# Kernel tuning notes

Measured on AMD Instinct MI355X. Metric: run time of the kernel, lower is better.

Reference implementation:

```python
import jax, jax.numpy as jnp
import numpy as np

N_SRC, N_DST, E, D, H = 100000, 10000, 320000, 128, 128
LN_EPS = 1e-5


def setup_inputs() -> dict:
    key = jax.random.key(0)
    ks = jax.random.split(key, 12)
    h_src = jax.random.normal(ks[0], (N_SRC, D), jnp.float32)
    h_dst = jax.random.normal(ks[1], (N_DST, D), jnp.float32)
    s_emb = jax.random.normal(ks[2], (N_DST, D), jnp.float32)
    edge_weight = jax.random.uniform(ks[3], (E,), jnp.float32)
    src_idx = jax.random.randint(ks[4], (E,), 0, N_SRC)
    dst_idx = jnp.sort(jax.random.randint(ks[5], (E,), 0, N_DST))
    # session_attention: Linear(2D->H, no bias) -> tanh -> Linear(H->1, no bias)
    W1 = jax.random.normal(ks[6], (2 * D, H), jnp.float32) / np.sqrt(2 * D)
    w2 = jax.random.normal(ks[7], (H,), jnp.float32) / np.sqrt(H)
    # output_proj: Linear(2D->D) with bias
    Wo = jax.random.normal(ks[8], (2 * D, D), jnp.float32) / np.sqrt(2 * D)
    bo = jnp.zeros((D,), jnp.float32)
    gamma = jnp.ones((D,), jnp.float32)
    beta = jnp.zeros((D,), jnp.float32)
    return {"h_src": h_src, "h_dst": h_dst, "s_emb": s_emb,
            "edge_weight": edge_weight, "src_idx": src_idx, "dst_idx": dst_idx,
            "W1": W1, "w2": w2, "Wo": Wo, "bo": bo, "gamma": gamma, "beta": beta}


def reference(h_src, h_dst, s_emb, edge_weight, src_idx, dst_idx, W1, w2, Wo, bo, gamma, beta):
    d = h_src.shape[1]
    # concat([h_src[src], s_emb[dst]]) @ W1 == h_src[src] @ W1[:d] + s_emb[dst] @ W1[d:]
    # project per-node first (cheaper than per-edge concat matmul)
    p_src = h_src @ W1[:d]          # [N_src, H]
    p_dst = s_emb @ W1[d:]          # [N_dst, H]
    raw = jnp.tanh(p_src[src_idx] + p_dst[dst_idx]) @ w2   # [E]
    raw = raw * edge_weight
    # edge_softmax: segment softmax over incoming edges of each dst node
    seg_max = jax.ops.segment_max(raw, dst_idx, num_segments=h_dst.shape[0])
    seg_max = jnp.where(jnp.isfinite(seg_max), seg_max, 0.0)  # handle degree-0 dsts
    ex = jnp.exp(raw - seg_max[dst_idx])
    den = jax.ops.segment_sum(ex, dst_idx, num_segments=h_dst.shape[0])
    attn = ex / den[dst_idx]                                 # [E]
    # u_mul_e + sum: weighted gather-scatter aggregation
    h_global = jax.ops.segment_sum(h_src[src_idx] * attn[:, None], dst_idx,
                                   num_segments=h_dst.shape[0])  # [N_dst, D]
    # output_proj on concat([h_dst, h_global])
    out = h_dst @ Wo[:d] + h_global @ Wo[d:] + bo
    # residual + layer norm (dropout = identity in eval)
    x = h_dst + out
    mu = jnp.mean(x, axis=-1, keepdims=True)
    var = jnp.mean((x - mu) ** 2, axis=-1, keepdims=True)
    y = (x - mu) / jnp.sqrt(var + LN_EPS) * gamma + beta
    return (y, attn[:, None])
```

## Files before the change

### kernel.cpp

```cpp
#include <hip/hip_runtime.h>
#include <math.h>

#define D128 128
#define SCAPW 256

typedef unsigned int uint32;
typedef unsigned short ushort_t;
typedef short bf16x8 __attribute__((ext_vector_type(8)));
typedef float f32x4 __attribute__((ext_vector_type(4)));

__device__ __forceinline__ ushort_t bf16_of(float x) {
  uint32 u = __float_as_uint(x);
  return (ushort_t)((u + 0x7fffu + ((u >> 16) & 1u)) >> 16);
}
__device__ __forceinline__ uint32 pack_bf2(float x, float y) {
  uint32 bx = __float_as_uint(x);
  uint32 by = __float_as_uint(y);
  bx = (bx + 0x7fffu + ((bx >> 16) & 1u)) >> 16;
  by = (by + 0x7fffu + ((by >> 16) & 1u)) & 0xffff0000u;
  return bx | by;
}
__device__ __forceinline__ float bf_lo(uint32 u) { return __uint_as_float(u << 16); }
__device__ __forceinline__ float bf_hi(uint32 u) { return __uint_as_float(u & 0xffff0000u); }

__device__ __forceinline__ float fast_tanh(float x) {
  float e = __expf(2.0f * x);
  float r = __builtin_amdgcn_rcpf(1.0f + e);
  return fmaf(-2.0f, r, 1.0f);
}

__global__ __launch_bounds__(256) void prep_all(
    const float* __restrict__ h_src, const float* __restrict__ s_emb,
    const float* __restrict__ h_dst,
    const float* __restrict__ W1, const float* __restrict__ Wo,
    const int* __restrict__ dst_idx,
    uint32* __restrict__ h_src_bf, uint32* __restrict__ s_emb_bf,
    uint32* __restrict__ h_dst_bf,
    ushort_t* __restrict__ Wfrag, ushort_t* __restrict__ Wo_frag,
    int* __restrict__ off,
    int n_src_el, int n_dst_el, int E, int N, int nb_conv) {
  const int b = blockIdx.x;
  const int tid = threadIdx.x;
  if (b < nb_conv) {
    int i = (b * 256 + tid) * 8;
    const int n_tot_el = n_src_el + 2 * n_dst_el;
    if (i >= n_tot_el) return;
    const float* src;
    uint32* dst;
    if (i < n_src_el) { src = h_src + i; dst = h_src_bf + (i >> 1); }
    else if (i < n_src_el + n_dst_el) {
      src = s_emb + (i - n_src_el); dst = s_emb_bf + ((i - n_src_el) >> 1);
    } else {
      src = h_dst + (i - n_src_el - n_dst_el);
      dst = h_dst_bf + ((i - n_src_el - n_dst_el) >> 1);
    }
    float4 a = *(const float4*)src;
    float4 c = *(const float4*)(src + 4);
    uint4 p;
    p.x = pack_bf2(a.x, a.y);
    p.y = pack_bf2(a.z, a.w);
    p.z = pack_bf2(c.x, c.y);
    p.w = pack_bf2(c.z, c.w);
    *(uint4*)dst = p;
  } else if (b < nb_conv + 16) {
    int t = (b - nb_conv) * 256 + tid;
    int lane = t & 63;
    int kc = (t >> 6) & 3;
    int nt = (t >> 8) & 7;
    int h = (t >> 11) & 1;
    int m = lane & 15;
    int quad = lane >> 4;
    int krow = h * D128 + kc * 32 + quad * 8;
    int ncol = nt * 16 + m;
    ushort_t fr[8];
#pragma unroll
    for (int j = 0; j < 8; j++) fr[j] = bf16_of(W1[(size_t)(krow + j) * D128 + ncol]);
    *(uint4*)(Wfrag + (size_t)t * 8) = *(const uint4*)fr;
  } else if (b < nb_conv + 32) {
    int t = (b - nb_conv - 16) * 256 + tid;
    int lane = t & 63;
    int kc = (t >> 6) & 7;
    int nt = (t >> 9) & 7;
    int m = lane & 15;
    int quad = lane >> 4;
    int krow = kc * 32 + quad * 8;
    int ncol = nt * 16 + m;
    ushort_t fr[8];
#pragma unroll
    for (int j = 0; j < 8; j++) fr[j] = bf16_of(Wo[(size_t)(krow + j) * D128 + ncol]);
    *(uint4*)(Wo_frag + (size_t)t * 8) = *(const uint4*)fr;
  } else {
    int e = (b - nb_conv - 32) * 256 + tid;
    if (e >= E) return;
    int d = dst_idx[e];
    int dprev = (e == 0) ? -1 : dst_idx[e - 1];
    for (int v = dprev + 1; v <= d; v++) off[v] = e;
    if (e == E - 1) {
      for (int v = d + 1; v <= N; v++) off[v] = E;
    }
  }
}

__global__ __launch_bounds__(256) void gemm_mfma(
    const ushort_t* __restrict__ Xa, const ushort_t* __restrict__ Xb,
    const ushort_t* __restrict__ Wfrag,
    ushort_t* __restrict__ Pa, ushort_t* __restrict__ Pb,
    int Ma, int Mb, int nblk_a) {
  __shared__ ushort_t Ys[128][132];
  const int blk = blockIdx.x;
  const ushort_t* X;
  const bf16x8* Wf;
  ushort_t* P;
  int M, row0;
  if (blk < nblk_a) { X = Xa; P = Pa; Wf = (const bf16x8*)Wfrag;           M = Ma; row0 = blk * 128; }
  else              { X = Xb; P = Pb; Wf = (const bf16x8*)(Wfrag + 16384); M = Mb; row0 = (blk - nblk_a) * 128; }

  const int tid = threadIdx.x;
  const int wave = tid >> 6;
  const int lane = tid & 63;
  const int m = lane & 15;
  const int quad = lane >> 4;

  const int ra0 = min(row0 + wave * 32 + m, M - 1);
  const int ra1 = min(row0 + wave * 32 + 16 + m, M - 1);

  f32x4 acc[2][8];
#pragma unroll
  for (int st = 0; st < 2; st++)
#pragma unroll
    for (int nt = 0; nt < 8; nt++) acc[st][nt] = (f32x4){0.f, 0.f, 0.f, 0.f};

#pragma unroll
  for (int kc = 0; kc < 4; kc++) {
    bf16x8 a0 = *(const bf16x8*)(X + (size_t)ra0 * D128 + kc * 32 + quad * 8);
    bf16x8 a1 = *(const bf16x8*)(X + (size_t)ra1 * D128 + kc * 32 + quad * 8);
#pragma unroll
    for (int nt = 0; nt < 8; nt++) {
      bf16x8 bfr = Wf[(nt * 4 + kc) * 64 + lane];
      acc[0][nt] = __builtin_amdgcn_mfma_f32_16x16x32_bf16(a0, bfr, acc[0][nt], 0, 0, 0);
      acc[1][nt] = __builtin_amdgcn_mfma_f32_16x16x32_bf16(a1, bfr, acc[1][nt], 0, 0, 0);
    }
  }

#pragma unroll
  for (int st = 0; st < 2; st++)
#pragma unroll
    for (int nt = 0; nt < 8; nt++)
#pragma unroll
      for (int r = 0; r < 4; r++)
        Ys[wave * 32 + st * 16 + quad * 4 + r][nt * 16 + m] = bf16_of(acc[st][nt][r]);
  __syncthreads();

#pragma unroll
  for (int it = 0; it < 16; it++) {
    int f = tid + 256 * it;
    int row = f >> 5;
    int c = (f & 31) * 4;
    int grow = row0 + row;
    if (grow < M) {
      uint2 v = *(const uint2*)(&Ys[row][c]);
      *(uint2*)(P + (size_t)grow * D128 + c) = v;
    }
  }
}

__global__ __launch_bounds__(256) void attn_agg_kernel(
    const uint32* __restrict__ p_src_bf, const uint32* __restrict__ p_dst_bf,
    const float* __restrict__ w2, const float* __restrict__ ew,
    const int* __restrict__ src_idx, const int* __restrict__ off,
    const uint32* __restrict__ h_src_bf2,
    float* __restrict__ attn_out, uint32* __restrict__ h_glob_bf, int N_dst) {
  const int tid = threadIdx.x;
  const int wv = tid >> 6;
  const int lane = tid & 63;
  const int v = blockIdx.x * 4 + wv;

  __shared__ float sw2[128];
  __shared__ float sex[4][SCAPW];
  __shared__ int ssrc[4][SCAPW];

  if (tid < 128) sw2[tid] = w2[tid];
  __syncthreads();
  if (v >= N_dst) return;

  const int lo = off[v], hi = off[v + 1];
  const int deg = hi - lo;
  const int sub = lane & 15;
  const int eg = lane >> 4;

  uint4 ud = *(const uint4*)(p_dst_bf + (size_t)v * 64 + sub * 4);
  float4 wA = *(const float4*)(&sw2[sub * 8]);
  float4 wB = *(const float4*)(&sw2[sub * 8 + 4]);

  float den = 0.f;
  float accx = 0.f, accy = 0.f;

  if (deg <= SCAPW) {
    for (int base = 0; base < deg; base += 4) {
      const int ei = base + eg;
      float acc = 0.f, ewv = 0.f;
      int s = 0;
      if (ei < deg) {
        const int e = lo + ei;
        s = src_idx[e];
        ewv = ew[e];
        uint4 us = *(const uint4*)(p_src_bf + (size_t)s * 64 + sub * 4);
        acc = fast_tanh(bf_lo(us.x) + bf_lo(ud.x)) * wA.x;
        acc = fmaf(fast_tanh(bf_hi(us.x) + bf_hi(ud.x)), wA.y, acc);
        acc = fmaf(fast_tanh(bf_lo(us.y) + bf_lo(ud.y)), wA.z, acc);
        acc = fmaf(fast_tanh(bf_hi(us.y) + bf_hi(ud.y)), wA.w, acc);
        acc = fmaf(fast_tanh(bf_lo(us.z) + bf_lo(ud.z)), wB.x, acc);
        acc = fmaf(fast_tanh(bf_hi(us.z) + bf_hi(ud.z)), wB.y, acc);
        acc = fmaf(fast_tanh(bf_lo(us.w) + bf_lo(ud.w)), wB.z, acc);
        acc = fmaf(fast_tanh(bf_hi(us.w) + bf_hi(ud.w)), wB.w, acc);
      }
#pragma unroll
      for (int o = 1; o <= 8; o <<= 1) acc += __shfl_xor(acc, o, 64);
      float ex = 0.f;
      if (ei < deg) {
        ex = __expf(acc * ewv);
        if (sub == 0) { sex[wv][ei] = ex; ssrc[wv][ei] = s; }
      }
      den += (sub == 0) ? ex : 0.f;
    }
    const int pad = (deg + 7) & ~7;
    for (int i = deg + lane; i < pad; i += 64) { sex[wv][i] = 0.f; ssrc[wv][i] = 0; }
#pragma unroll
    for (int o = 1; o <= 32; o <<= 1) den += __shfl_xor(den, o, 64);
    const float inv = (deg > 0) ? 1.0f / den : 0.0f;

    for (int i = lane; i < deg; i += 64) attn_out[lo + i] = sex[wv][i] * inv;

    const int nb = pad >> 3;
    for (int b = 0; b < nb; b++) {
      const int base = b * 8;
#pragma unroll
      for (int j = 0; j < 8; j++) {
        float ex = sex[wv][base + j];
        int s = ssrc[wv][base + j];
        uint32 u = h_src_bf2[(size_t)s * 64 + lane];
        accx = fmaf(ex, bf_lo(u), accx);
        accy = fmaf(ex, bf_hi(u), accy);
      }
    }
    h_glob_bf[(size_t)v * 64 + lane] = pack_bf2(accx * inv, accy * inv);
  } else {
    for (int base = 0; base < deg; base += 4) {
      const int ei = base + eg;
      float acc = 0.f, ewv = 0.f;
      if (ei < deg) {
        const int e = lo + ei;
        int s = src_idx[e];
        ewv = ew[e];
        uint4 us = *(const uint4*)(p_src_bf + (size_t)s * 64 + sub * 4);
        acc = fast_tanh(bf_lo(us.x) + bf_lo(ud.x)) * wA.x;
        acc = fmaf(fast_tanh(bf_hi(us.x) + bf_hi(ud.x)), wA.y, acc);
        acc = fmaf(fast_tanh(bf_lo(us.y) + bf_lo(ud.y)), wA.z, acc);
        acc = fmaf(fast_tanh(bf_hi(us.y) + bf_hi(ud.y)), wA.w, acc);
        acc = fmaf(fast_tanh(bf_lo(us.z) + bf_lo(ud.z)), wB.x, acc);
        acc = fmaf(fast_tanh(bf_hi(us.z) + bf_hi(ud.z)), wB.y, acc);
        acc = fmaf(fast_tanh(bf_lo(us.w) + bf_lo(ud.w)), wB.z, acc);
        acc = fmaf(fast_tanh(bf_hi(us.w) + bf_hi(ud.w)), wB.w, acc);
      }
#pragma unroll
      for (int o = 1; o <= 8; o <<= 1) acc += __shfl_xor(acc, o, 64);
      float ex = 0.f;
      if (ei < deg) {
        ex = __expf(acc * ewv);
        if (sub == 0) attn_out[lo + ei] = ex;
      }
      den += (sub == 0) ? ex : 0.f;
    }
#pragma unroll
    for (int o = 1; o <= 32; o <<= 1) den += __shfl_xor(den, o, 64);
    const float inv = 1.0f / den;

    for (int i0 = 0; i0 < deg; i0 += 8) {
#pragma unroll
      for (int j = 0; j < 8; j++) {
        const int i = i0 + j;
        float ex = 0.f;
        int s = 0;
        if (i < deg) { ex = attn_out[lo + i]; s = src_idx[lo + i]; }
        uint32 u = h_src_bf2[(size_t)s * 64 + lane];
        accx = fmaf(ex, bf_lo(u), accx);
        accy = fmaf(ex, bf_hi(u), accy);
        if (i < deg && lane == 0) attn_out[lo + i] = ex * inv;
      }
    }
    h_glob_bf[(size_t)v * 64 + lane] = pack_bf2(accx * inv, accy * inv);
  }
}

__global__ __launch_bounds__(128) void out_mfma_ln(
    const ushort_t* __restrict__ h_dst_bf, const ushort_t* __restrict__ h_glob_bf,
    const ushort_t* __restrict__ Wo_frag,
    const float* __restrict__ h_dst, const float* __restrict__ bo,
    const float* __restrict__ gamma, const float* __restrict__ beta,
    float* __restrict__ y, int N) {
  __shared__ float sbo[128], sgam[128], sbet[128];
  const int tid = threadIdx.x;
  if (tid < 128) { sbo[tid] = bo[tid]; sgam[tid] = gamma[tid]; sbet[tid] = beta[tid]; }
  __syncthreads();

  const int w = tid >> 6;
  const int lane = tid & 63;
  const int m = lane & 15;
  const int quad = lane >> 4;
  const int row0 = blockIdx.x * 32 + w * 16;
  const int ra = min(row0 + m, N - 1);
  const bf16x8* Wf = (const bf16x8*)Wo_frag;

  f32x4 acc[8];
#pragma unroll
  for (int nt = 0; nt < 8; nt++) acc[nt] = (f32x4){0.f, 0.f, 0.f, 0.f};

#pragma unroll
  for (int kc = 0; kc < 8; kc++) {
    const ushort_t* X = (kc < 4) ? h_dst_bf : h_glob_bf;
    const int kk = kc & 3;
    bf16x8 a = *(const bf16x8*)(X + (size_t)ra * D128 + kk * 32 + quad * 8);
#pragma unroll
    for (int nt = 0; nt < 8; nt++) {
      bf16x8 bfr = Wf[(nt * 8 + kc) * 64 + lane];
      acc[nt] = __builtin_amdgcn_mfma_f32_16x16x32_bf16(a, bfr, acc[nt], 0, 0, 0);
    }
  }

#pragma unroll
  for (int r = 0; r < 4; r++) {
    const int grow = row0 + quad * 4 + r;
    const int gr = min(grow, N - 1);
    float x[8];
    float s1 = 0.f, s2 = 0.f;
#pragma unroll
    for (int nt = 0; nt < 8; nt++) {
      float hd = h_dst[(size_t)gr * D128 + nt * 16 + m];
      float xv = hd + acc[nt][r] + sbo[nt * 16 + m];
      x[nt] = xv;
      s1 += xv;
      s2 = fmaf(xv, xv, s2);
    }
#pragma unroll
    for (int o = 1; o <= 8; o <<= 1) {
      s1 += __shfl_xor(s1, o, 64);
      s2 += __shfl_xor(s2, o, 64);
    }
    float mu = s1 * (1.0f / 128.0f);
    float var = s2 * (1.0f / 128.0f) - mu * mu;
    float rstd = __builtin_amdgcn_rcpf(sqrtf(var + 1e-5f));
    if (grow < N) {
#pragma unroll
      for (int nt = 0; nt < 8; nt++) {
        int c = nt * 16 + m;
        y[(size_t)grow * D128 + c] = (x[nt] - mu) * rstd * sgam[c] + sbet[c];
      }
    }
  }
}

extern "C" void kernel_launch(void* const* d_in, const int* in_sizes, int n_in,
                              void* d_out, int out_size, void* d_ws, size_t ws_size,
                              hipStream_t stream) {
  const float* h_src = (const float*)d_in[0];
  const float* h_dst = (const float*)d_in[1];
  const float* s_emb = (const float*)d_in[2];
  const float* ew    = (const float*)d_in[3];
  const int* src_idx = (const int*)d_in[4];
  const int* dst_idx = (const int*)d_in[5];
  const float* W1    = (const float*)d_in[6];
  const float* w2    = (const float*)d_in[7];
  const float* Wo    = (const float*)d_in[8];
  const float* bo    = (const float*)d_in[9];
  const float* gamma = (const float*)d_in[10];
  const float* beta  = (const float*)d_in[11];

  const int N_src = in_sizes[0] / D128;
  const int N_dst = in_sizes[1] / D128;
  const int E = in_sizes[3];

  float* out_y = (float*)d_out;
  float* out_attn = out_y + (size_t)N_dst * D128;

  uint32* p_src_bf = (uint32*)d_ws;
  uint32* p_dst_bf = p_src_bf + (size_t)N_src * 64;
  uint32* h_src_bf = p_dst_bf + (size_t)N_dst * 64;
  uint32* h_dst_bf = h_src_bf + (size_t)N_src * 64;
  uint32* h_glob_bf = h_dst_bf + (size_t)N_dst * 64;
  uint32* s_emb_bf = h_glob_bf + (size_t)N_dst * 64;
  int* seg_off = (int*)(s_emb_bf + (size_t)N_dst * 64);
  ushort_t* Wfrag = (ushort_t*)(seg_off + N_dst + 1 + 3);
  ushort_t* Wo_frag = Wfrag + 32768;

  const int n_src_el = N_src * D128;
  const int n_dst_el = N_dst * D128;
  const int n_tot_el = n_src_el + 2 * n_dst_el;
  const int nblk_a = (N_src + 127) / 128;
  const int nblk_b = (N_dst + 127) / 128;
  const int nb_conv = (n_tot_el / 8 + 255) / 256;
  const int nb_seg = (E + 255) / 256;

  prep_all<<<nb_conv + 32 + nb_seg, 256, 0, stream>>>(
      h_src, s_emb, h_dst, W1, Wo, dst_idx,
      h_src_bf, s_emb_bf, h_dst_bf, Wfrag, Wo_frag, seg_off,
      n_src_el, n_dst_el, E, N_dst, nb_conv);
  gemm_mfma<<<nblk_a + nblk_b, 256, 0, stream>>>(
      (const ushort_t*)h_src_bf, (const ushort_t*)s_emb_bf, Wfrag,
      (ushort_t*)p_src_bf, (ushort_t*)p_dst_bf, N_src, N_dst, nblk_a);
  attn_agg_kernel<<<(N_dst + 3) / 4, 256, 0, stream>>>(
      p_src_bf, p_dst_bf, w2, ew, src_idx, seg_off, h_src_bf, out_attn,
      h_glob_bf, N_dst);
  out_mfma_ln<<<(N_dst + 31) / 32, 128, 0, stream>>>(
      (const ushort_t*)h_dst_bf, (const ushort_t*)h_glob_bf, Wo_frag,
      h_dst, bo, gamma, beta, out_y, N_dst);
}
```

Before: 176.4 us.

## Store projections and gathered features in fp8 and fuse aggregation into score loop

The per-node projections p_src/p_dst and an extra copy of h_src are now stored as fp8. The GEMM swaps its MFMA operands so each lane can pack four outputs into one fp8 word. The attention kernel reads the fp8 rows and accumulates the weighted h_src sum in the same pass that computes scores, dropping the second gather loop and the LDS staging of source indices. This cuts gather bytes on the edge-bound kernel, but adds an fp8 conversion pass over h_src in prep and lowers precision, which may hurt accuracy.

```diff
diff --git a/kernel.cpp b/kernel.cpp
--- a/kernel.cpp
+++ b/kernel.cpp
@@ -8,6 +8,7 @@
 typedef unsigned short ushort_t;
 typedef short bf16x8 __attribute__((ext_vector_type(8)));
 typedef float f32x4 __attribute__((ext_vector_type(4)));
+typedef float f32x2 __attribute__((ext_vector_type(2)));
 
 __device__ __forceinline__ ushort_t bf16_of(float x) {
   uint32 u = __float_as_uint(x);
@@ -29,13 +30,19 @@
   return fmaf(-2.0f, r, 1.0f);
 }
 
+__device__ __forceinline__ uint32 pack_fp8x4(float a, float b, float c, float d) {
+  int u = __builtin_amdgcn_cvt_pk_fp8_f32(a, b, 0, false);
+  u = __builtin_amdgcn_cvt_pk_fp8_f32(c, d, u, true);
+  return (uint32)u;
+}
+
 __global__ __launch_bounds__(256) void prep_all(
     const float* __restrict__ h_src, const float* __restrict__ s_emb,
     const float* __restrict__ h_dst,
     const float* __restrict__ W1, const float* __restrict__ Wo,
     const int* __restrict__ dst_idx,
     uint32* __restrict__ h_src_bf, uint32* __restrict__ s_emb_bf,
-    uint32* __restrict__ h_dst_bf,
+    uint32* __restrict__ h_dst_bf, uint32* __restrict__ h_src_f8,
     ushort_t* __restrict__ Wfrag, ushort_t* __restrict__ Wo_frag,
     int* __restrict__ off,
     int n_src_el, int n_dst_el, int E, int N, int nb_conv) {
@@ -43,25 +50,35 @@
   const int tid = threadIdx.x;
   if (b < nb_conv) {
     int i = (b * 256 + tid) * 8;
-    const int n_tot_el = n_src_el + 2 * n_dst_el;
-    if (i >= n_tot_el) return;
-    const float* src;
-    uint32* dst;
-    if (i < n_src_el) { src = h_src + i; dst = h_src_bf + (i >> 1); }
-    else if (i < n_src_el + n_dst_el) {
-      src = s_emb + (i - n_src_el); dst = s_emb_bf + ((i - n_src_el) >> 1);
+    const int n_bf_el = n_src_el + 2 * n_dst_el;
+    if (i < n_bf_el) {
+      const float* src;
+      uint32* dst;
+      if (i < n_src_el) { src = h_src + i; dst = h_src_bf + (i >> 1); }
+      else if (i < n_src_el + n_dst_el) {
+        src = s_emb + (i - n_src_el); dst = s_emb_bf + ((i - n_src_el) >> 1);
+      } else {
+        src = h_dst + (i - n_src_el - n_dst_el);
+        dst = h_dst_bf + ((i - n_src_el - n_dst_el) >> 1);
+      }
+      float4 a = *(const float4*)src;
+      float4 c = *(const float4*)(src + 4);
+      uint4 p;
+      p.x = pack_bf2(a.x, a.y);
+      p.y = pack_bf2(a.z, a.w);
+      p.z = pack_bf2(c.x, c.y);
+      p.w = pack_bf2(c.z, c.w);
+      *(uint4*)dst = p;
     } else {
-      src = h_dst + (i - n_src_el - n_dst_el);
-      dst = h_dst_bf + ((i - n_src_el - n_dst_el) >> 1);
-    }
-    float4 a = *(const float4*)src;
-    float4 c = *(const float4*)(src + 4);
-    uint4 p;
-    p.x = pack_bf2(a.x, a.y);
-    p.y = pack_bf2(a.z, a.w);
-    p.z = pack_bf2(c.x, c.y);
-    p.w = pack_bf2(c.z, c.w);
-    *(uint4*)dst = p;
+      int k = i - n_bf_el;
+      if (k >= n_src_el) return;
+      float4 a = *(const float4*)(h_src + k);
+      float4 c = *(const float4*)(h_src + k + 4);
+      uint2 p;
+      p.x = pack_fp8x4(a.x, a.y, a.z, a.w);
+      p.y = pack_fp8x4(c.x, c.y, c.z, c.w);
+      *(uint2*)(h_src_f8 + (k >> 2)) = p;
+    }
   } else if (b < nb_conv + 16) {
     int t = (b - nb_conv) * 256 + tid;
     int lane = t & 63;
@@ -104,13 +121,13 @@
 __global__ __launch_bounds__(256) void gemm_mfma(
     const ushort_t* __restrict__ Xa, const ushort_t* __restrict__ Xb,
     const ushort_t* __restrict__ Wfrag,
-    ushort_t* __restrict__ Pa, ushort_t* __restrict__ Pb,
+    uint32* __restrict__ Pa, uint32* __restrict__ Pb,
     int Ma, int Mb, int nblk_a) {
-  __shared__ ushort_t Ys[128][132];
+  __shared__ uint32 Ys8[128][36];
   const int blk = blockIdx.x;
   const ushort_t* X;
   const bf16x8* Wf;
-  ushort_t* P;
+  uint32* P;
   int M, row0;
   if (blk < nblk_a) { X = Xa; P = Pa; Wf = (const bf16x8*)Wfrag;           M = Ma; row0 = blk * 128; }
   else              { X = Xb; P = Pb; Wf = (const bf16x8*)(Wfrag + 16384); M = Mb; row0 = (blk - nblk_a) * 128; }
@@ -132,13 +149,13 @@
 
 #pragma unroll
   for (int kc = 0; kc < 4; kc++) {
-    bf16x8 a0 = *(const bf16x8*)(X + (size_t)ra0 * D128 + kc * 32 + quad * 8);
-    bf16x8 a1 = *(const bf16x8*)(X + (size_t)ra1 * D128 + kc * 32 + quad * 8);
+    bf16x8 x0 = *(const bf16x8*)(X + (size_t)ra0 * D128 + kc * 32 + quad * 8);
+    bf16x8 x1 = *(const bf16x8*)(X + (size_t)ra1 * D128 + kc * 32 + quad * 8);
 #pragma unroll
     for (int nt = 0; nt < 8; nt++) {
-      bf16x8 bfr = Wf[(nt * 4 + kc) * 64 + lane];
-      acc[0][nt] = __builtin_amdgcn_mfma_f32_16x16x32_bf16(a0, bfr, acc[0][nt], 0, 0, 0);
-      acc[1][nt] = __builtin_amdgcn_mfma_f32_16x16x32_bf16(a1, bfr, acc[1][nt], 0, 0, 0);
+      bf16x8 wf = Wf[(nt * 4 + kc) * 64 + lane];
+      acc[0][nt] = __builtin_amdgcn_mfma_f32_16x16x32_bf16(wf, x0, acc[0][nt], 0, 0, 0);
+      acc[1][nt] = __builtin_amdgcn_mfma_f32_16x16x32_bf16(wf, x1, acc[1][nt], 0, 0, 0);
     }
   }
 
@@ -146,149 +163,120 @@
   for (int st = 0; st < 2; st++)
 #pragma unroll
     for (int nt = 0; nt < 8; nt++)
-#pragma unroll
-      for (int r = 0; r < 4; r++)
-        Ys[wave * 32 + st * 16 + quad * 4 + r][nt * 16 + m] = bf16_of(acc[st][nt][r]);
+      Ys8[wave * 32 + st * 16 + m][nt * 4 + quad] =
+          pack_fp8x4(acc[st][nt][0], acc[st][nt][1], acc[st][nt][2], acc[st][nt][3]);
   __syncthreads();
 
 #pragma unroll
-  for (int it = 0; it < 16; it++) {
+  for (int it = 0; it < 4; it++) {
     int f = tid + 256 * it;
-    int row = f >> 5;
-    int c = (f & 31) * 4;
+    int row = f >> 3;
+    int cu = (f & 7) * 4;
     int grow = row0 + row;
-    if (grow < M) {
-      uint2 v = *(const uint2*)(&Ys[row][c]);
-      *(uint2*)(P + (size_t)grow * D128 + c) = v;
-    }
+    if (grow < M) *(uint4*)(P + (size_t)grow * 32 + cu) = *(const uint4*)(&Ys8[row][cu]);
   }
 }
 
 __global__ __launch_bounds__(256) void attn_agg_kernel(
-    const uint32* __restrict__ p_src_bf, const uint32* __restrict__ p_dst_bf,
+    const uint32* __restrict__ p_src_f8, const uint32* __restrict__ p_dst_f8,
     const float* __restrict__ w2, const float* __restrict__ ew,
     const int* __restrict__ src_idx, const int* __restrict__ off,
-    const uint32* __restrict__ h_src_bf2,
+    const uint32* __restrict__ h_src_f8,
     float* __restrict__ attn_out, uint32* __restrict__ h_glob_bf, int N_dst) {
   const int tid = threadIdx.x;
   const int wv = tid >> 6;
   const int lane = tid & 63;
   const int v = blockIdx.x * 4 + wv;
 
-  __shared__ float sw2[128];
   __shared__ float sex[4][SCAPW];
-  __shared__ int ssrc[4][SCAPW];
-
-  if (tid < 128) sw2[tid] = w2[tid];
-  __syncthreads();
   if (v >= N_dst) return;
 
   const int lo = off[v], hi = off[v + 1];
   const int deg = hi - lo;
   const int sub = lane & 15;
   const int eg = lane >> 4;
-
-  uint4 ud = *(const uint4*)(p_dst_bf + (size_t)v * 64 + sub * 4);
-  float4 wA = *(const float4*)(&sw2[sub * 8]);
-  float4 wB = *(const float4*)(&sw2[sub * 8 + 4]);
+  const bool fast = (deg <= SCAPW);
+
+  float4 wA = *(const float4*)(w2 + sub * 8);
+  float4 wB = *(const float4*)(w2 + sub * 8 + 4);
+  uint2 pdu = *(const uint2*)(p_dst_f8 + (size_t)v * 32 + sub * 2);
+  f32x2 pd0 = __builtin_amdgcn_cvt_pk_f32_fp8(pdu.x, false);
+  f32x2 pd1 = __builtin_amdgcn_cvt_pk_f32_fp8(pdu.x, true);
+  f32x2 pd2 = __builtin_amdgcn_cvt_pk_f32_fp8(pdu.y, false);
+  f32x2 pd3 = __builtin_amdgcn_cvt_pk_f32_fp8(pdu.y, true);
 
   float den = 0.f;
-  float accx = 0.f, accy = 0.f;
-
-  if (deg <= SCAPW) {
-    for (int base = 0; base < deg; base += 4) {
-      const int ei = base + eg;
-      float acc = 0.f, ewv = 0.f;
-      int s = 0;
-      if (ei < deg) {
-        const int e = lo + ei;
-        s = src_idx[e];
-        ewv = ew[e];
-        uint4 us = *(const uint4*)(p_src_bf + (size_t)s * 64 + sub * 4);
-        acc = fast_tanh(bf_lo(us.x) + bf_lo(ud.x)) * wA.x;
-        acc = fmaf(fast_tanh(bf_hi(us.x) + bf_hi(ud.x)), wA.y, acc);
-        acc = fmaf(fast_tanh(bf_lo(us.y) + bf_lo(ud.y)), wA.z, acc);
-        acc = fmaf(fast_tanh(bf_hi(us.y) + bf_hi(ud.y)), wA.w, acc);
-        acc = fmaf(fast_tanh(bf_lo(us.z) + bf_lo(ud.z)), wB.x, acc);
-        acc = fmaf(fast_tanh(bf_hi(us.z) + bf_hi(ud.z)), wB.y, acc);
-        acc = fmaf(fast_tanh(bf_lo(us.w) + bf_lo(ud.w)), wB.z, acc);
-        acc = fmaf(fast_tanh(bf_hi(us.w) + bf_hi(ud.w)), wB.w, acc);
+  float acc[8];
+#pragma unroll
+  for (int j = 0; j < 8; j++) acc[j] = 0.f;
+
+  for (int base = 0; base < deg; base += 4) {
+    const int ei = base + eg;
+    float ex = 0.f;
+    if (ei < deg) {
+      const int e = lo + ei;
+      const int s = src_idx[e];
+      const float ewv = ew[e];
+      uint2 us = *(const uint2*)(p_src_f8 + (size_t)s * 32 + sub * 2);
+      f32x2 a0 = __builtin_amdgcn_cvt_pk_f32_fp8(us.x, false);
+      f32x2 a1 = __builtin_amdgcn_cvt_pk_f32_fp8(us.x, true);
+      f32x2 a2 = __builtin_amdgcn_cvt_pk_f32_fp8(us.y, false);
+      f32x2 a3 = __builtin_amdgcn_cvt_pk_f32_fp8(us.y, true);
+      float sc;
+      sc = fast_tanh(a0.x + pd0.x) * wA.x;
+      sc = fmaf(fast_tanh(a0.y + pd0.y), wA.y, sc);
+      sc = fmaf(fast_tanh(a1.x + pd1.x), wA.z, sc);
+      sc = fmaf(fast_tanh(a1.y + pd1.y), wA.w, sc);
+      sc = fmaf(fast_tanh(a2.x + pd2.x), wB.x, sc);
+      sc = fmaf(fast_tanh(a2.y + pd2.y), wB.y, sc);
+      sc = fmaf(fast_tanh(a3.x + pd3.x), wB.z, sc);
+      sc = fmaf(fast_tanh(a3.y + pd3.y), wB.w, sc);
+#pragma unroll
+      for (int o = 1; o <= 8; o <<= 1) sc += __shfl_xor(sc, o, 64);
+      ex = __expf(sc * ewv);
+      if (sub == 0) {
+        if (fast) sex[wv][ei] = ex;
+        else attn_out[lo + ei] = ex;
       }
-#pragma unroll
-      for (int o = 1; o <= 8; o <<= 1) acc += __shfl_xor(acc, o, 64);
-      float ex = 0.f;
-      if (ei < deg) {
-        ex = __expf(acc * ewv);
-        if (sub == 0) { sex[wv][ei] = ex; ssrc[wv][ei] = s; }
-      }
-      den += (sub == 0) ? ex : 0.f;
-    }
-    const int pad = (deg + 7) & ~7;
-    for (int i = deg + lane; i < pad; i += 64) { sex[wv][i] = 0.f; ssrc[wv][i] = 0; }
-#pragma unroll
-    for (int o = 1; o <= 32; o <<= 1) den += __shfl_xor(den, o, 64);
-    const float inv = (deg > 0) ? 1.0f / den : 0.0f;
-
+      uint2 uh = *(const uint2*)(h_src_f8 + (size_t)s * 32 + sub * 2);
+      f32x2 h0 = __builtin_amdgcn_cvt_pk_f32_fp8(uh.x, false);
+      f32x2 h1 = __builtin_amdgcn_cvt_pk_f32_fp8(uh.x, true);
+      f32x2 h2 = __builtin_amdgcn_cvt_pk_f32_fp8(uh.y, false);
+      f32x2 h3 = __builtin_amdgcn_cvt_pk_f32_fp8(uh.y, true);
+      acc[0] = fmaf(ex, h0.x, acc[0]);
+      acc[1] = fmaf(ex, h0.y, acc[1]);
+      acc[2] = fmaf(ex, h1.x, acc[2]);
+      acc[3] = fmaf(ex, h1.y, acc[3]);
+      acc[4] = fmaf(ex, h2.x, acc[4]);
+      acc[5] = fmaf(ex, h2.y, acc[5]);
+      acc[6] = fmaf(ex, h3.x, acc[6]);
+      acc[7] = fmaf(ex, h3.y, acc[7]);
+    }
+    den += (sub == 0) ? ex : 0.f;
+  }
+
+#pragma unroll
+  for (int o = 1; o <= 32; o <<= 1) den += __shfl_xor(den, o, 64);
+  const float inv = (deg > 0) ? 1.0f / den : 0.0f;
+
+  if (fast) {
     for (int i = lane; i < deg; i += 64) attn_out[lo + i] = sex[wv][i] * inv;
-
-    const int nb = pad >> 3;
-    for (int b = 0; b < nb; b++) {
-      const int base = b * 8;
-#pragma unroll
-      for (int j = 0; j < 8; j++) {
-        float ex = sex[wv][base + j];
-        int s = ssrc[wv][base + j];
-        uint32 u = h_src_bf2[(size_t)s * 64 + lane];
-        accx = fmaf(ex, bf_lo(u), accx);
-        accy = fmaf(ex, bf_hi(u), accy);
-      }
-    }
-    h_glob_bf[(size_t)v * 64 + lane] = pack_bf2(accx * inv, accy * inv);
   } else {
-    for (int base = 0; base < deg; base += 4) {
-      const int ei = base + eg;
-      float acc = 0.f, ewv = 0.f;
-      if (ei < deg) {
-        const int e = lo + ei;
-        int s = src_idx[e];
-        ewv = ew[e];
-        uint4 us = *(const uint4*)(p_src_bf + (size_t)s * 64 + sub * 4);
-        acc = fast_tanh(bf_lo(us.x) + bf_lo(ud.x)) * wA.x;
-        acc = fmaf(fast_tanh(bf_hi(us.x) + bf_hi(ud.x)), wA.y, acc);
-        acc = fmaf(fast_tanh(bf_lo(us.y) + bf_lo(ud.y)), wA.z, acc);
-        acc = fmaf(fast_tanh(bf_hi(us.y) + bf_hi(ud.y)), wA.w, acc);
-        acc = fmaf(fast_tanh(bf_lo(us.z) + bf_lo(ud.z)), wB.x, acc);
-        acc = fmaf(fast_tanh(bf_hi(us.z) + bf_hi(ud.z)), wB.y, acc);
-        acc = fmaf(fast_tanh(bf_lo(us.w) + bf_lo(ud.w)), wB.z, acc);
-        acc = fmaf(fast_tanh(bf_hi(us.w) + bf_hi(ud.w)), wB.w, acc);
-      }
-#pragma unroll
-      for (int o = 1; o <= 8; o <<= 1) acc += __shfl_xor(acc, o, 64);
-      float ex = 0.f;
-      if (ei < deg) {
-        ex = __expf(acc * ewv);
-        if (sub == 0) attn_out[lo + ei] = ex;
-      }
-      den += (sub == 0) ? ex : 0.f;
-    }
-#pragma unroll
-    for (int o = 1; o <= 32; o <<= 1) den += __shfl_xor(den, o, 64);
-    const float inv = 1.0f / den;
-
-    for (int i0 = 0; i0 < deg; i0 += 8) {
-#pragma unroll
-      for (int j = 0; j < 8; j++) {
-        const int i = i0 + j;
-        float ex = 0.f;
-        int s = 0;
-        if (i < deg) { ex = attn_out[lo + i]; s = src_idx[lo + i]; }
-        uint32 u = h_src_bf2[(size_t)s * 64 + lane];
-        accx = fmaf(ex, bf_lo(u), accx);
-        accy = fmaf(ex, bf_hi(u), accy);
-        if (i < deg && lane == 0) attn_out[lo + i] = ex * inv;
-      }
-    }
-    h_glob_bf[(size_t)v * 64 + lane] = pack_bf2(accx * inv, accy * inv);
+    for (int i = lane; i < deg; i += 64) attn_out[lo + i] *= inv;
+  }
+
+#pragma unroll
+  for (int j = 0; j < 8; j++) {
+    acc[j] += __shfl_xor(acc[j], 16, 64);
+    acc[j] += __shfl_xor(acc[j], 32, 64);
+  }
+  if (eg == 0) {
+    uint4 o;
+    o.x = pack_bf2(acc[0] * inv, acc[1] * inv);
+    o.y = pack_bf2(acc[2] * inv, acc[3] * inv);
+    o.z = pack_bf2(acc[4] * inv, acc[5] * inv);
+    o.w = pack_bf2(acc[6] * inv, acc[7] * inv);
+    *(uint4*)(h_glob_bf + (size_t)v * 64 + sub * 4) = o;
   }
 }
 
@@ -382,9 +370,10 @@
   float* out_y = (float*)d_out;
   float* out_attn = out_y + (size_t)N_dst * D128;
 
-  uint32* p_src_bf = (uint32*)d_ws;
-  uint32* p_dst_bf = p_src_bf + (size_t)N_src * 64;
-  uint32* h_src_bf = p_dst_bf + (size_t)N_dst * 64;
+  uint32* p_src_f8 = (uint32*)d_ws;
+  uint32* p_dst_f8 = p_src_f8 + (size_t)N_src * 32;
+  uint32* h_src_f8 = p_dst_f8 + (size_t)N_dst * 32;
+  uint32* h_src_bf = h_src_f8 + (size_t)N_src * 32;
   uint32* h_dst_bf = h_src_bf + (size_t)N_src * 64;
   uint32* h_glob_bf = h_dst_bf + (size_t)N_dst * 64;
   uint32* s_emb_bf = h_glob_bf + (size_t)N_dst * 64;
@@ -394,21 +383,21 @@
 
   const int n_src_el = N_src * D128;
   const int n_dst_el = N_dst * D128;
-  const int n_tot_el = n_src_el + 2 * n_dst_el;
+  const int n_conv_el = 2 * n_src_el + 2 * n_dst_el;
   const int nblk_a = (N_src + 127) / 128;
   const int nblk_b = (N_dst + 127) / 128;
-  const int nb_conv = (n_tot_el / 8 + 255) / 256;
+  const int nb_conv = (n_conv_el / 8 + 255) / 256;
   const int nb_seg = (E + 255) / 256;
 
   prep_all<<<nb_conv + 32 + nb_seg, 256, 0, stream>>>(
       h_src, s_emb, h_dst, W1, Wo, dst_idx,
-      h_src_bf, s_emb_bf, h_dst_bf, Wfrag, Wo_frag, seg_off,
+      h_src_bf, s_emb_bf, h_dst_bf, h_src_f8, Wfrag, Wo_frag, seg_off,
       n_src_el, n_dst_el, E, N_dst, nb_conv);
   gemm_mfma<<<nblk_a + nblk_b, 256, 0, stream>>>(
       (const ushort_t*)h_src_bf, (const ushort_t*)s_emb_bf, Wfrag,
-      (ushort_t*)p_src_bf, (ushort_t*)p_dst_bf, N_src, N_dst, nblk_a);
+      p_src_f8, p_dst_f8, N_src, N_dst, nblk_a);
   attn_agg_kernel<<<(N_dst + 3) / 4, 256, 0, stream>>>(
-      p_src_bf, p_dst_bf, w2, ew, src_idx, seg_off, h_src_bf, out_attn,
+      p_src_f8, p_dst_f8, w2, ew, src_idx, seg_off, h_src_f8, out_attn,
       h_glob_bf, N_dst);
   out_mfma_ln<<<(N_dst + 31) / 32, 128, 0, stream>>>(
       (const ushort_t*)h_dst_bf, (const ushort_t*)h_glob_bf, Wo_frag,
```

New measurement: 181.8 us. +3.0%, slower.
